# Kernel optimization log

Hardware: AMD Instinct MI355X
Metric: run time of the kernel (lower is better)

Reference implementation:

```python
import jax, jax.numpy as jnp
import numpy as np

B, L, H, A = 2, 1024, 768, 12          # batch, doc_len, hidden, attn heads
E, M, P = 24, 8, 552                   # entities/doc, mentions/entity, entity pairs/doc
EMB, BLK, NL = 768, 64, 97             # emb_size, block_size, num relation labels
OFFSET = 1                             # [CLS] offset


def setup_inputs() -> dict:
    key = jax.random.key(0)
    ks = jax.random.split(key, 16)
    w = lambda k, shape: (jax.random.normal(k, shape, jnp.float32) * 0.02)
    return {
        'sequence_output': jax.random.normal(ks[0], (B, L, H), jnp.float32),
        'attention': jax.random.uniform(ks[1], (B, A, L, L), jnp.float32),
        'mention_mask': jnp.ones((B, E, M), jnp.float32),
        'Wh': w(ks[2], (2 * H, EMB)),  'bh': jnp.zeros((EMB,), jnp.float32),
        'Wt': w(ks[3], (2 * H, EMB)),  'bt': jnp.zeros((EMB,), jnp.float32),
        'Wh2': w(ks[4], (3 * H, EMB)), 'bh2': jnp.zeros((EMB,), jnp.float32),
        'Wt2': w(ks[5], (3 * H, EMB)), 'bt2': jnp.zeros((EMB,), jnp.float32),
        'W2': w(ks[6], (EMB * BLK, H)), 'b2': jnp.zeros((H,), jnp.float32),
        'Wb': w(ks[7], (EMB * BLK, NL)), 'bb': jnp.zeros((NL,), jnp.float32),
        'mention_idx': jax.random.randint(ks[8], (B, E, M), 0, L - OFFSET),
        'hts': jax.random.randint(ks[9], (B, P, 2), 0, E),
    }


def _block_bilinear(a, b):
    # grouped (block) bilinear: [N, EMB] x [N, EMB] -> [N, EMB*BLK]
    b1 = a.reshape(-1, EMB // BLK, BLK)
    b2 = b.reshape(-1, EMB // BLK, BLK)
    return jnp.einsum('nkb,nkc->nkbc', b1, b2).reshape(-1, EMB * BLK)


def reference(sequence_output, attention, mention_mask,
              Wh, bh, Wt, bt, Wh2, bh2, Wt2, bt2, W2, b2, Wb, bb,
              mention_idx, hts):
    bidx = jnp.arange(B)[:, None, None]
    pos = mention_idx + OFFSET                              # [B,E,M]

    # --- get_hrt: ragged mention gather + logsumexp / mean pooling ---
    ment_emb = sequence_output[bidx, pos]                   # [B,E,M,H]
    mm = mention_mask[..., None]
    x = jnp.where(mm > 0, ment_emb, -1e30)
    mx = x.max(axis=2, keepdims=True)
    ent_emb = (mx + jnp.log(jnp.sum(jnp.exp(x - mx), axis=2, keepdims=True))).squeeze(2)  # [B,E,H]

    ment_att = attention[bidx, :, pos]                      # [B,E,M,A,L]
    cnt = jnp.clip(mention_mask.sum(-1), 1.0)[:, :, None, None]
    ent_att = (ment_att * mention_mask[..., None, None]).sum(2) / cnt  # [B,E,A,L]

    bidx2 = jnp.arange(B)[:, None]
    hs = ent_emb[bidx2, hts[..., 0]]                        # [B,P,H]
    ts = ent_emb[bidx2, hts[..., 1]]
    h_att = ent_att[bidx2, hts[..., 0]]                     # [B,P,A,L]
    t_att = ent_att[bidx2, hts[..., 1]]
    ht_att = (h_att * t_att).mean(2)                        # [B,P,L]
    ht_att = ht_att / (ht_att.sum(-1, keepdims=True) + 1e-30)
    rs = jnp.einsum('bpl,blh->bph', ht_att, sequence_output)  # localized context

    hs = hs.reshape(-1, H); ts = ts.reshape(-1, H); rs = rs.reshape(-1, H)

    # --- forward_rel: extractors + grouped block-bilinear scoring ---
    hs1 = jnp.tanh(jnp.concatenate([hs, rs], -1) @ Wh + bh)
    ts1 = jnp.tanh(jnp.concatenate([ts, rs], -1) @ Wt + bt)
    hts_feat = _block_bilinear(hs1, ts1) @ W2 + b2          # [N,H]
    hs2 = jnp.tanh(jnp.concatenate([hs1, rs, hts_feat], -1) @ Wh2 + bh2)
    ts2 = jnp.tanh(jnp.concatenate([ts1, rs, hts_feat], -1) @ Wt2 + bt2)
    logits = _block_bilinear(hs2, ts2) @ Wb + bb            # [N,NL]
    return logits
```

## Files before the change

### kernel.cpp

```cpp
#include <hip/hip_runtime.h>
#include <hip/hip_bf16.h>

#define B_ 2
#define L_ 1024
#define H_ 768
#define A_ 12
#define E_ 24
#define M_ 8
#define P_ 552
#define EMB_ 768
#define BLK_ 64
#define NBLK_ 12
#define NL_ 97
#define NP_ (B_*P_)
#define KTOT_ 49152
#define TP_ 8
#define NC_ 8

typedef float f32x4 __attribute__((ext_vector_type(4)));
typedef _Float16 f16x8 __attribute__((ext_vector_type(8)));

static __device__ __forceinline__ unsigned short f2h(float f){
    _Float16 h = (_Float16)f;
    unsigned short u; __builtin_memcpy(&u, &h, 2); return u;
}

static __device__ __forceinline__ void gload_lds16(const unsigned short* g, unsigned short* l){
    __builtin_amdgcn_global_load_lds(
        (const __attribute__((address_space(1))) unsigned int*)(const void*)g,
        (__attribute__((address_space(3))) unsigned int*)(void*)l, 16, 0, 0);
}

__global__ void k_ent_emb(const float* __restrict__ seq, const float* __restrict__ mask,
                          const int* __restrict__ midx, float* __restrict__ ent_emb)
{
    int be = blockIdx.x;
    int b = be / E_;
    int h = threadIdx.x;
    float v[M_];
    float mx = -1e30f;
    #pragma unroll
    for (int m = 0; m < M_; ++m) {
        float w = mask[be*M_ + m];
        int p = midx[be*M_ + m] + 1;
        float x = (w > 0.f) ? seq[(b*L_ + p)*H_ + h] : -1e30f;
        v[m] = x; mx = fmaxf(mx, x);
    }
    float s = 0.f;
    #pragma unroll
    for (int m = 0; m < M_; ++m) s += expf(v[m] - mx);
    ent_emb[be*H_ + h] = mx + logf(s);
}

__global__ void k_ent_att(const float* __restrict__ att, const float* __restrict__ mask,
                          const int* __restrict__ midx, float* __restrict__ ent_att)
{
    int bea = blockIdx.x;
    int a = bea % A_;
    int be = bea / A_;
    int b = be / E_;
    float cnt = 0.f;
    #pragma unroll
    for (int m = 0; m < M_; ++m) cnt += mask[be*M_ + m];
    cnt = fmaxf(cnt, 1.f);
    float inv = 1.f / cnt;
    for (int l = threadIdx.x; l < L_; l += blockDim.x) {
        float acc = 0.f;
        #pragma unroll
        for (int m = 0; m < M_; ++m) {
            float w = mask[be*M_ + m];
            if (w > 0.f) {
                int p = midx[be*M_ + m] + 1;
                acc += w * att[((size_t)(b*A_ + a)*L_ + p)*L_ + l];
            }
        }
        ent_att[(size_t)(be*A_ + a)*L_ + l] = acc * inv;
    }
}

__global__ void k_ht_att(const float* __restrict__ ent_att, const int* __restrict__ hts,
                         float* __restrict__ ht_att)
{
    int bp = blockIdx.x;
    int b = bp / P_;
    int he = hts[bp*2 + 0];
    int te = hts[bp*2 + 1];
    const float* ha = ent_att + (size_t)(b*E_ + he)*A_*L_;
    const float* ta = ent_att + (size_t)(b*E_ + te)*A_*L_;
    __shared__ float red[256];
    float lsum = 0.f;
    for (int l = threadIdx.x; l < L_; l += 256) {
        float q = 0.f;
        #pragma unroll
        for (int a = 0; a < A_; ++a) q += ha[a*L_ + l] * ta[a*L_ + l];
        q *= (1.f / A_);
        ht_att[(size_t)bp*L_ + l] = q;
        lsum += q;
    }
    red[threadIdx.x] = lsum;
    __syncthreads();
    for (int s = 128; s > 0; s >>= 1) {
        if (threadIdx.x < s) red[threadIdx.x] += red[threadIdx.x + s];
        __syncthreads();
    }
    float scale = 1.f / (red[0] + 1e-30f);
    for (int l = threadIdx.x; l < L_; l += 256)
        ht_att[(size_t)bp*L_ + l] *= scale;
}

__global__ void k_wt_multi(const float* __restrict__ W2, unsigned short* __restrict__ w2t,
                           const float* __restrict__ seq, unsigned short* __restrict__ seqT)
{
    int t = blockIdx.x;
    const float* in; unsigned short* out; int K, N, kt, ct;
    if (t < 9216)       { in = W2;              out = w2t;             K = KTOT_; N = 768; kt = t % 768; ct = t / 768; }
    else if (t < 9408)  { t -= 9216; in = seq;                 out = seqT;              K = L_; N = 768; kt = t % 16; ct = t / 16; }
    else                { t -= 9408; in = seq + (size_t)L_*H_; out = seqT + (size_t)768*L_; K = L_; N = 768; kt = t % 16; ct = t / 16; }
    __shared__ float tl[64][65];
    int k0 = kt*64, c0 = ct*64;
    int tx = threadIdx.x & 63, ty = threadIdx.x >> 6;
    #pragma unroll
    for (int q = 0; q < 16; ++q) {
        int r = ty*16 + q;
        tl[r][tx] = in[(size_t)(k0 + r)*N + c0 + tx];
    }
    __syncthreads();
    #pragma unroll
    for (int q = 0; q < 16; ++q) {
        int col = ty*16 + q;
        out[(size_t)(c0+col)*K + k0 + tx] = f2h(tl[tx][col]);
    }
}

__global__ void k_wt_f16(const float* __restrict__ in, unsigned short* __restrict__ out,
                         int K, int N, int Npad)
{
    __shared__ float t[64][65];
    int k0 = blockIdx.x*64, c0 = blockIdx.y*64;
    int tx = threadIdx.x & 63, ty = threadIdx.x >> 6;
    #pragma unroll
    for (int q = 0; q < 16; ++q) {
        int r = ty*16 + q;
        float v = 0.f;
        if (c0 + tx < N) v = in[(size_t)(k0 + r)*N + c0 + tx];
        t[r][tx] = v;
    }
    __syncthreads();
    #pragma unroll
    for (int q = 0; q < 16; ++q) {
        int col = ty*16 + q;
        if (c0 + col < Npad) out[(size_t)(c0+col)*K + k0 + tx] = f2h(t[tx][col]);
    }
}

__global__ void k_wt_f16x2(const float* __restrict__ in0, unsigned short* __restrict__ out0,
                           const float* __restrict__ in1, unsigned short* __restrict__ out1,
                           int K, int N, int Npad)
{
    const float* in = blockIdx.z ? in1 : in0;
    unsigned short* out = blockIdx.z ? out1 : out0;
    __shared__ float t[64][65];
    int k0 = blockIdx.x*64, c0 = blockIdx.y*64;
    int tx = threadIdx.x & 63, ty = threadIdx.x >> 6;
    #pragma unroll
    for (int q = 0; q < 16; ++q) {
        int r = ty*16 + q;
        float v = 0.f;
        if (c0 + tx < N) v = in[(size_t)(k0 + r)*N + c0 + tx];
        t[r][tx] = v;
    }
    __syncthreads();
    #pragma unroll
    for (int q = 0; q < 16; ++q) {
        int col = ty*16 + q;
        if (c0 + col < Npad) out[(size_t)(c0+col)*K + k0 + tx] = f2h(t[tx][col]);
    }
}

__launch_bounds__(256, 3)
__global__ void k_rs_mfma(const float* __restrict__ ht_att, const unsigned short* __restrict__ seqT,
                          float* __restrict__ Cpart)
{
    __shared__ _Float16 Ash[128][64];
    __shared__ _Float16 Bsh[128][64];
    int tid = threadIdx.x;
    int lane = tid & 63, wid = tid >> 6;
    int wr = (wid >> 1)*64, wc = (wid & 1)*64;
    int r16 = lane & 15, g = lane >> 4;
    int z = blockIdx.z;
    int b = z >> 3, kc = z & 7;
    int c0 = blockIdx.x*128;
    int row0 = blockIdx.y*128;
    const float* At = ht_att + (size_t)b*P_*L_;
    const unsigned short* Bt = seqT + (size_t)b*768*L_;
    int srccol = (lane >> 3);
    int srcch  = (lane & 7) ^ (srccol & 7);

    f32x4 acc[4][4];
    #pragma unroll
    for (int a = 0; a < 4; ++a)
        #pragma unroll
        for (int bq = 0; bq < 4; ++bq) acc[a][bq] = (f32x4){0.f,0.f,0.f,0.f};

    for (int s = 0; s < 2; ++s) {
        __syncthreads();
        #pragma unroll
        for (int q = 0; q < 4; ++q) {
            int idx = q*256 + tid;
            int row = idx >> 3, ch = idx & 7;
            int p = row0 + row; if (p >= P_) p = P_ - 1;
            const float* pp = &At[(size_t)p*L_ + kc*128 + s*64 + ch*8];
            f32x4 a0 = *(const f32x4*)pp;
            f32x4 a1 = *(const f32x4*)(pp + 4);
            f16x8 h;
            h[0]=(_Float16)a0[0]; h[1]=(_Float16)a0[1]; h[2]=(_Float16)a0[2]; h[3]=(_Float16)a0[3];
            h[4]=(_Float16)a1[0]; h[5]=(_Float16)a1[1]; h[6]=(_Float16)a1[2]; h[7]=(_Float16)a1[3];
            *(f16x8*)&Ash[row][(ch ^ (row & 7))*8] = h;
        }
        #pragma unroll
        for (int q = 0; q < 4; ++q) {
            int colb = (q*4 + wid)*8;
            int col = colb + srccol;
            gload_lds16(&Bt[(size_t)(c0+col)*L_ + kc*128 + s*64 + srcch*8],
                        (unsigned short*)&Bsh[colb][0]);
        }
        __syncthreads();
        #pragma unroll
        for (int kk = 0; kk < 2; ++kk) {
            f16x8 bfr[4];
            #pragma unroll
            for (int ni = 0; ni < 4; ++ni)
                bfr[ni] = *(f16x8*)&Bsh[wc + ni*16 + r16][((kk*4 + g) ^ (r16 & 7))*8];
            #pragma unroll
            for (int mi = 0; mi < 4; ++mi) {
                f16x8 afr = *(f16x8*)&Ash[wr + mi*16 + r16][((kk*4 + g) ^ (r16 & 7))*8];
                #pragma unroll
                for (int ni = 0; ni < 4; ++ni)
                    acc[mi][ni] = __builtin_amdgcn_mfma_f32_16x16x32_f16(afr, bfr[ni], acc[mi][ni], 0, 0, 0);
            }
        }
    }

    #pragma unroll
    for (int mi = 0; mi < 4; ++mi)
      #pragma unroll
      for (int ni = 0; ni < 4; ++ni)
        #pragma unroll
        for (int r = 0; r < 4; ++r) {
            int p = row0 + wr + mi*16 + g*4 + r;
            if (p < P_)
                Cpart[((size_t)kc*NP_ + b*P_ + p)*768 + c0 + wc + ni*16 + r16] = acc[mi][ni][r];
        }
}

__global__ void k_rs_reduce(const float* __restrict__ rspart, float* __restrict__ rs)
{
    int idx = blockIdx.x*256 + threadIdx.x;
    if (idx >= NP_*768/4) return;
    f32x4 s = {0.f,0.f,0.f,0.f};
    #pragma unroll
    for (int z = 0; z < NC_; ++z) s += *(const f32x4*)&rspart[(size_t)z*NP_*768 + (size_t)idx*4];
    *(f32x4*)&rs[(size_t)idx*4] = s;
}

__global__ void k_rs(const float* __restrict__ seq, const float* __restrict__ ht_att,
                     float* __restrict__ rs)
{
    int blk = blockIdx.x;
    int b = blk / (P_/TP_);
    int p0 = (blk % (P_/TP_)) * TP_;
    const float* sq = seq + (size_t)b*L_*H_;
    float acc[TP_][3];
    #pragma unroll
    for (int t = 0; t < TP_; ++t)
        #pragma unroll
        for (int c = 0; c < 3; ++c) acc[t][c] = 0.f;
    for (int l = 0; l < L_; ++l) {
        float w[TP_];
        #pragma unroll
        for (int t = 0; t < TP_; ++t) w[t] = ht_att[(size_t)(b*P_ + p0 + t)*L_ + l];
        #pragma unroll
        for (int c = 0; c < 3; ++c) {
            float v = sq[(size_t)l*H_ + threadIdx.x + 256*c];
            #pragma unroll
            for (int t = 0; t < TP_; ++t) acc[t][c] += w[t]*v;
        }
    }
    #pragma unroll
    for (int t = 0; t < TP_; ++t)
        #pragma unroll
        for (int c = 0; c < 3; ++c)
            rs[(size_t)(b*P_ + p0 + t)*H_ + threadIdx.x + 256*c] = acc[t][c];
}

__global__ void k_gather(const float* __restrict__ ent_emb, const int* __restrict__ hts,
                         float* __restrict__ hs, float* __restrict__ ts)
{
    int bp = blockIdx.x;
    int b = bp / P_;
    int he = hts[bp*2 + 0];
    int te = hts[bp*2 + 1];
    int h = threadIdx.x;
    hs[(size_t)bp*H_ + h] = ent_emb[(b*E_ + he)*H_ + h];
    ts[(size_t)bp*H_ + h] = ent_emb[(b*E_ + te)*H_ + h];
}

__global__ void k_gemm_reduce_tanh2(const float* __restrict__ gpA, const float* __restrict__ gpB,
                                    const float* __restrict__ biasA, const float* __restrict__ biasB,
                                    float* __restrict__ CA, float* __restrict__ CB, int nz)
{
    const float* Cpart = blockIdx.y ? gpB : gpA;
    const float* bias  = blockIdx.y ? biasB : biasA;
    float* C           = blockIdx.y ? CB : CA;
    int idx = blockIdx.x*256 + threadIdx.x;
    if (idx >= NP_*768/4) return;
    int c4 = (idx*4) % 768;
    f32x4 s = *(const f32x4*)&bias[c4];
    for (int z = 0; z < nz; ++z) s += *(const f32x4*)&Cpart[(size_t)z*NP_*768 + (size_t)idx*4];
    f32x4 r;
    #pragma unroll
    for (int j = 0; j < 4; ++j) r[j] = tanhf(s[j]);
    *(f32x4*)&C[(size_t)idx*4] = r;
}

template<int NPARTS, bool DOTANH>
__global__ void k_gemm_concat(const float* __restrict__ A0, const float* __restrict__ A1,
                              const float* __restrict__ A2, const float* __restrict__ W,
                              const float* __restrict__ bias, float* __restrict__ C,
                              int Mrows)
{
    const int BK = 16;
    __shared__ float As[BK][64];
    __shared__ float Bs[BK][64];
    int tid = threadIdx.x;
    int ty = tid >> 4, tx = tid & 15;
    int by = blockIdx.y, bx = blockIdx.x;
    float acc[4][4] = {};
    const int K = NPARTS * 768;
    for (int kk0 = 0; kk0 < K; kk0 += BK) {
        const float* Ap = (kk0 < 768) ? A0 : ((NPARTS >= 3 && kk0 >= 1536) ? A2 : A1);
        int klocal = kk0 % 768;
        {
            int idx = tid * 4;
            int r = idx >> 4;
            int k = idx & 15;
            int row = by*64 + r;
            float4 v = make_float4(0.f,0.f,0.f,0.f);
            if (row < Mrows) v = *(const float4*)(Ap + (size_t)row*768 + klocal + k);
            As[k+0][r] = v.x; As[k+1][r] = v.y; As[k+2][r] = v.z; As[k+3][r] = v.w;
        }
        {
            int idx = tid * 4;
            int k = idx >> 6;
            int c = idx & 63;
            *(float4*)&Bs[k][c] = *(const float4*)(W + (size_t)(kk0 + k)*768 + bx*64 + c);
        }
        __syncthreads();
        #pragma unroll
        for (int k = 0; k < BK; ++k) {
            float a4[4], b4[4];
            *(float4*)a4 = *(float4*)&As[k][ty*4];
            *(float4*)b4 = *(float4*)&Bs[k][tx*4];
            #pragma unroll
            for (int i = 0; i < 4; ++i)
                #pragma unroll
                for (int j = 0; j < 4; ++j) acc[i][j] += a4[i]*b4[j];
        }
        __syncthreads();
    }
    #pragma unroll
    for (int i = 0; i < 4; ++i) {
        int row = by*64 + ty*4 + i;
        if (row >= Mrows) continue;
        #pragma unroll
        for (int j = 0; j < 4; ++j) {
            int col = bx*64 + tx*4 + j;
            float v = acc[i][j] + bias[col];
            if (DOTANH) v = tanhf(v);
            C[(size_t)row*768 + col] = v;
        }
    }
}

template<int NSTEP, bool GATHER0>
__launch_bounds__(256, 3)
__global__ void k_gemm_mfma2(const float* __restrict__ A0a, const float* __restrict__ A0b,
                             const float* __restrict__ A1, const float* __restrict__ A2,
                             const int* __restrict__ hts,
                             const unsigned short* __restrict__ WTa, const unsigned short* __restrict__ WTb,
                             float* __restrict__ Cpa, float* __restrict__ Cpb,
                             int Mrows, int Ktot, int partdiv, int nzhalf)
{
    __shared__ _Float16 Ash[128][64];
    __shared__ _Float16 Bsh[128][64];
    int tid = threadIdx.x;
    int lane = tid & 63, wid = tid >> 6;
    int wr = (wid >> 1)*64, wc = (wid & 1)*64;
    int r16 = lane & 15, g = lane >> 4;
    int zz = blockIdx.z;
    int half = zz / nzhalf;
    int z = zz % nzhalf;
    const unsigned short* WT = half ? WTb : WTa;
    float* Cpart = half ? Cpb : Cpa;
    int part = z / partdiv, chunk = z % partdiv;
    int ka = chunk * (NSTEP*64);
    int kb = part*768 + ka;
    const float* A = (part == 0) ? (half ? A0b : A0a) : ((part == 1) ? A1 : A2);
    int c0 = blockIdx.x*128;
    int row0 = blockIdx.y*128;
    int srccol = (lane >> 3);
    int srcch  = (lane & 7) ^ (srccol & 7);

    f32x4 acc[4][4];
    #pragma unroll
    for (int a = 0; a < 4; ++a)
        #pragma unroll
        for (int b = 0; b < 4; ++b) acc[a][b] = (f32x4){0.f,0.f,0.f,0.f};

    for (int s = 0; s < NSTEP; ++s) {
        __syncthreads();
        #pragma unroll
        for (int q = 0; q < 4; ++q) {
            int idx = q*256 + tid;
            int row = idx >> 3, ch = idx & 7;
            int grow = row0 + row; if (grow >= Mrows) grow = Mrows - 1;
            const float* p;
            if (GATHER0 && part == 0) {
                int bb_ = grow / P_;
                int e = hts[grow*2 + half];
                p = &A0a[((size_t)(bb_*E_ + e))*768 + ka + s*64 + ch*8];
            } else {
                p = &A[(size_t)grow*768 + ka + s*64 + ch*8];
            }
            f32x4 a0 = *(const f32x4*)p;
            f32x4 a1 = *(const f32x4*)(p + 4);
            f16x8 h;
            h[0]=(_Float16)a0[0]; h[1]=(_Float16)a0[1]; h[2]=(_Float16)a0[2]; h[3]=(_Float16)a0[3];
            h[4]=(_Float16)a1[0]; h[5]=(_Float16)a1[1]; h[6]=(_Float16)a1[2]; h[7]=(_Float16)a1[3];
            *(f16x8*)&Ash[row][(ch ^ (row & 7))*8] = h;
        }
        #pragma unroll
        for (int q = 0; q < 4; ++q) {
            int colb = (q*4 + wid)*8;
            int col = colb + srccol;
            gload_lds16(&WT[(size_t)(c0+col)*Ktot + kb + s*64 + srcch*8],
                        (unsigned short*)&Bsh[colb][0]);
        }
        __syncthreads();
        #pragma unroll
        for (int kk = 0; kk < 2; ++kk) {
            f16x8 bfr[4];
            #pragma unroll
            for (int ni = 0; ni < 4; ++ni)
                bfr[ni] = *(f16x8*)&Bsh[wc + ni*16 + r16][((kk*4 + g) ^ (r16 & 7))*8];
            #pragma unroll
            for (int mi = 0; mi < 4; ++mi) {
                f16x8 afr = *(f16x8*)&Ash[wr + mi*16 + r16][((kk*4 + g) ^ (r16 & 7))*8];
                #pragma unroll
                for (int ni = 0; ni < 4; ++ni)
                    acc[mi][ni] = __builtin_amdgcn_mfma_f32_16x16x32_f16(afr, bfr[ni], acc[mi][ni], 0, 0, 0);
            }
        }
    }

    #pragma unroll
    for (int mi = 0; mi < 4; ++mi)
      #pragma unroll
      for (int ni = 0; ni < 4; ++ni)
        #pragma unroll
        for (int r = 0; r < 4; ++r) {
            int row = row0 + wr + mi*16 + g*4 + r;
            if (row < Mrows)
                Cpart[((size_t)z*Mrows + row)*768 + c0 + wc + ni*16 + r16] = acc[mi][ni][r];
        }
}

template<int ILEN, bool SWZ>
__launch_bounds__(256, 3)
__global__ void k_bb_mfma(const float* __restrict__ U, const float* __restrict__ V,
                          const unsigned short* __restrict__ BT, float* __restrict__ Cpart,
                          int Mrows, int ldc)
{
    const int ISPLIT = 64 / ILEN;
    __shared__ unsigned short Ush[128][ILEN + 2];
    __shared__ _Float16 Bs[2][128][64];
    int tid = threadIdx.x;
    int lane = tid & 63, wid = tid >> 6;
    int wr = (wid >> 1)*64, wc = (wid & 1)*64;
    int r16 = lane & 15, g = lane >> 4;
    int bx = blockIdx.x, by = blockIdx.y, z = blockIdx.z;
    if (SWZ) {
        int h = bx + 6*by + 54*z;
        int x = h & 7, j = h >> 3;
        int p = x*9 + j/9;
        by = j % 9;
        bx = p % 6;
        z  = p / 6;
    }
    int kz = z / ISPLIT, si = z % ISPLIT;
    int ibeg = si * ILEN;
    int c0 = bx*128;
    int row0 = by*128;
    int srccol = (lane >> 3);
    int srcch  = (lane & 7) ^ (srccol & 7);
    const unsigned short* BTkz = BT + (size_t)kz*4096;

    #pragma unroll
    for (int q = 0; q < (128*ILEN)/1024; ++q) {
        int idx = (q*256 + tid)*4;
        int r = idx / ILEN, c = idx % ILEN;
        int row = row0 + r; if (row >= Mrows) row = Mrows - 1;
        f32x4 v = *(const f32x4*)&U[(size_t)row*EMB_ + kz*64 + ibeg + c];
        Ush[r][c+0] = f2h(v[0]); Ush[r][c+1] = f2h(v[1]);
        Ush[r][c+2] = f2h(v[2]); Ush[r][c+3] = f2h(v[3]);
    }
    f16x8 vfh[2][4];
    #pragma unroll
    for (int kk = 0; kk < 2; ++kk)
      #pragma unroll
      for (int mi = 0; mi < 4; ++mi) {
        int row = row0 + wr + mi*16 + r16; if (row >= Mrows) row = Mrows - 1;
        const float* p = &V[(size_t)row*EMB_ + kz*64 + kk*32 + g*8];
        f16x8 t;
        #pragma unroll
        for (int e = 0; e < 8; ++e) t[e] = (_Float16)p[e];
        vfh[kk][mi] = t;
      }
    #pragma unroll
    for (int q = 0; q < 4; ++q) {
        int colb = (q*4 + wid)*8;
        int col = colb + srccol;
        gload_lds16(&BTkz[(size_t)(c0+col)*KTOT_ + (size_t)ibeg*64 + srcch*8],
                    (unsigned short*)&Bs[0][colb][0]);
    }
    __syncthreads();

    f32x4 acc[4][4];
    #pragma unroll
    for (int a = 0; a < 4; ++a)
        #pragma unroll
        for (int b = 0; b < 4; ++b) acc[a][b] = (f32x4){0.f,0.f,0.f,0.f};

    for (int ii = 0; ii < ILEN; ++ii) {
        int cur = ii & 1, nxt = cur ^ 1;
        if (ii < ILEN-1) {
            #pragma unroll
            for (int q = 0; q < 4; ++q) {
                int colb = (q*4 + wid)*8;
                int col = colb + srccol;
                gload_lds16(&BTkz[(size_t)(c0+col)*KTOT_ + (size_t)(ibeg+ii+1)*64 + srcch*8],
                            (unsigned short*)&Bs[nxt][colb][0]);
            }
        }
        f16x8 u8[4];
        #pragma unroll
        for (int mi = 0; mi < 4; ++mi) {
            unsigned short ub = Ush[wr + mi*16 + r16][ii];
            _Float16 uh; __builtin_memcpy(&uh, &ub, 2);
            #pragma unroll
            for (int e = 0; e < 8; ++e) u8[mi][e] = uh;
        }
        #pragma unroll
        for (int kk = 0; kk < 2; ++kk) {
            f16x8 bfr[4];
            #pragma unroll
            for (int ni = 0; ni < 4; ++ni) {
                int row = wc + ni*16 + r16;
                bfr[ni] = *(f16x8*)&Bs[cur][row][((kk*4 + g) ^ (r16 & 7))*8];
            }
            #pragma unroll
            for (int mi = 0; mi < 4; ++mi) {
                f16x8 afr = u8[mi] * vfh[kk][mi];
                #pragma unroll
                for (int ni = 0; ni < 4; ++ni)
                    acc[mi][ni] = __builtin_amdgcn_mfma_f32_16x16x32_f16(afr, bfr[ni], acc[mi][ni], 0, 0, 0);
            }
        }
        __syncthreads();
    }

    #pragma unroll
    for (int mi = 0; mi < 4; ++mi)
      #pragma unroll
      for (int ni = 0; ni < 4; ++ni)
        #pragma unroll
        for (int r = 0; r < 4; ++r) {
            int row = row0 + wr + mi*16 + g*4 + r;
            if (row < Mrows)
                Cpart[((size_t)z*Mrows + row)*ldc + c0 + wc + ni*16 + r16] = acc[mi][ni][r];
        }
}

__global__ void k_reduce_feat(const float* __restrict__ part, const float* __restrict__ bias,
                              float* __restrict__ out)
{
    int idx = blockIdx.x*256 + threadIdx.x;
    if (idx >= (NP_*768)/4) return;
    int c4 = (idx*4) % 768;
    f32x4 s = *(const f32x4*)&bias[c4];
    #pragma unroll
    for (int z = 0; z < NBLK_; ++z) s += *(const f32x4*)&part[(size_t)z*NP_*768 + (size_t)idx*4];
    *(f32x4*)&out[(size_t)idx*4] = s;
}

__global__ void k_reduce_logits(const float* __restrict__ part, const float* __restrict__ bb,
                                float* __restrict__ out, int nz)
{
    int idx = blockIdx.x*256 + threadIdx.x;
    if (idx >= NP_*NL_) return;
    int n = idx / NL_, c = idx % NL_;
    float s = bb[c];
    for (int z = 0; z < nz; ++z) s += part[(size_t)z*NP_*128 + (size_t)n*128 + c];
    out[idx] = s;
}

template<bool GUARD, bool SPLITK>
__global__ void k_bbgemm(const float* __restrict__ U, const float* __restrict__ V,
                         const float* __restrict__ W, const float* __restrict__ bias,
                         float* __restrict__ C, int Mrows, int Ncols, int ldw, int ldc)
{
    __shared__ float Us[64][68];
    __shared__ float Vs[64][68];
    __shared__ float Bsh[16][64];
    int tid = threadIdx.x;
    int ty = tid >> 4, tx = tid & 15;
    int by = blockIdx.y, bx = blockIdx.x;
    int c0 = bx*64;
    float acc[4][4] = {};
    int kbeg = SPLITK ? blockIdx.z : 0;
    int kend = SPLITK ? blockIdx.z + 1 : NBLK_;
    for (int k = kbeg; k < kend; ++k) {
        #pragma unroll
        for (int e = 0; e < 4; ++e) {
            int idx = (e*256 + tid)*4;
            int r = idx >> 6, c = idx & 63;
            int row = by*64 + r;
            float4 u = make_float4(0.f,0.f,0.f,0.f), vv = make_float4(0.f,0.f,0.f,0.f);
            if (row < Mrows) {
                u  = *(const float4*)(U + (size_t)row*EMB_ + k*BLK_ + c);
                vv = *(const float4*)(V + (size_t)row*EMB_ + k*BLK_ + c);
            }
            *(float4*)&Us[r][c] = u;
            *(float4*)&Vs[r][c] = vv;
        }
        __syncthreads();
        for (int t = 0; t < 256; ++t) {
            int i = t >> 2;
            int jb = (t & 3) * 16;
            {
                int idx = tid * 4;
                int kk = idx >> 6, c = idx & 63;
                size_t wrow = (size_t)(k*256 + t)*16 + kk;
                if (GUARD) {
                    #pragma unroll
                    for (int q = 0; q < 4; ++q) {
                        int col = c0 + c + q;
                        Bsh[kk][c+q] = (col < Ncols) ? W[wrow*ldw + col] : 0.f;
                    }
                } else {
                    *(float4*)&Bsh[kk][c] = *(const float4*)(W + wrow*ldw + c0 + c);
                }
            }
            __syncthreads();
            float u[4];
            #pragma unroll
            for (int r = 0; r < 4; ++r) u[r] = Us[ty*4+r][i];
            #pragma unroll
            for (int kk = 0; kk < 16; ++kk) {
                float b4[4];
                *(float4*)b4 = *(float4*)&Bsh[kk][tx*4];
                #pragma unroll
                for (int r = 0; r < 4; ++r) {
                    float a = u[r] * Vs[ty*4+r][jb+kk];
                    #pragma unroll
                    for (int j = 0; j < 4; ++j) acc[r][j] += a*b4[j];
                }
            }
            __syncthreads();
        }
    }
    #pragma unroll
    for (int r = 0; r < 4; ++r) {
        int row = by*64 + ty*4 + r;
        if (row >= Mrows) continue;
        #pragma unroll
        for (int j = 0; j < 4; ++j) {
            int col = c0 + tx*4 + j;
            if (GUARD && col >= Ncols) continue;
            float v = acc[r][j];
            if (!SPLITK) v += bias[col];
            size_t out_idx = SPLITK ? ((size_t)(blockIdx.z*Mrows + row)*ldc + col)
                                    : ((size_t)row*ldc + col);
            C[out_idx] = v;
        }
    }
}

__global__ void k_logits_reduce_old(const float* __restrict__ part, const float* __restrict__ bb,
                                    float* __restrict__ out)
{
    int idx = blockIdx.x*256 + threadIdx.x;
    if (idx >= NP_*NL_) return;
    int col = idx % NL_;
    float s = bb[col];
    #pragma unroll
    for (int z = 0; z < NBLK_; ++z) s += part[(size_t)z*NP_*NL_ + idx];
    out[idx] = s;
}

extern "C" void kernel_launch(void* const* d_in, const int* in_sizes, int n_in,
                              void* d_out, int out_size, void* d_ws, size_t ws_size,
                              hipStream_t stream)
{
    (void)in_sizes; (void)n_in; (void)out_size;
    const float* seq  = (const float*)d_in[0];
    const float* att  = (const float*)d_in[1];
    const float* mask = (const float*)d_in[2];
    const float* Wh   = (const float*)d_in[3];
    const float* bh   = (const float*)d_in[4];
    const float* Wt   = (const float*)d_in[5];
    const float* bt   = (const float*)d_in[6];
    const float* Wh2  = (const float*)d_in[7];
    const float* bh2  = (const float*)d_in[8];
    const float* Wt2  = (const float*)d_in[9];
    const float* bt2  = (const float*)d_in[10];
    const float* W2   = (const float*)d_in[11];
    const float* b2   = (const float*)d_in[12];
    const float* Wb   = (const float*)d_in[13];
    const float* bb   = (const float*)d_in[14];
    const int* midx   = (const int*)d_in[15];
    const int* hts    = (const int*)d_in[16];
    float* out = (float*)d_out;
    float* ws  = (float*)d_ws;

    float* ent_emb = ws;
    float* ent_att = ent_emb + 36864;
    float* ht_att  = ent_att + 589824;
    float* rs      = ht_att + 1130496;
    float* hs      = rs   + 847872;
    float* ts      = hs   + 847872;
    float* hs1     = ts   + 847872;
    float* ts1     = hs1  + 847872;
    float* feat    = ts1  + 847872;
    float* hs2     = feat + 847872;
    float* ts2     = hs2  + 847872;
    float* featpart = ts2 + 847872;
    float* spare    = featpart + 10174464;
    unsigned short* w2t = (unsigned short*)(spare + 1695744);
    unsigned short* Rrgn = (unsigned short*)(spare + 1695744 + 18874368);
    const size_t need_bytes = (size_t)42430464 * 4;
    const bool use_mfma = (ws_size >= need_bytes);

    unsigned short* whT  = Rrgn;
    unsigned short* wtT  = Rrgn + 1179648;
    unsigned short* wh2T = Rrgn;
    unsigned short* wt2T = Rrgn + 1769472;
    unsigned short* wbt  = Rrgn;

    unsigned short* seqT = (unsigned short*)hs;

    float* rspart  = featpart;
    float* gpA     = featpart;
    float* gpB     = featpart + 5087232;
    float* logpart = featpart;

    k_ent_emb<<<dim3(B_*E_), dim3(H_), 0, stream>>>(seq, mask, midx, ent_emb);
    k_ent_att<<<dim3(B_*E_*A_), dim3(256), 0, stream>>>(att, mask, midx, ent_att);
    k_ht_att<<<dim3(NP_), dim3(256), 0, stream>>>(ent_att, hts, ht_att);

    if (use_mfma) {
        k_wt_multi<<<dim3(9600), dim3(256), 0, stream>>>(W2, w2t, seq, seqT);

        k_rs_mfma<<<dim3(6, 5, 16), dim3(256), 0, stream>>>(ht_att, seqT, rspart);
        k_rs_reduce<<<dim3(828), dim3(256), 0, stream>>>(rspart, rs);

        k_wt_f16x2<<<dim3(1536/64, 768/64, 2), dim3(256), 0, stream>>>(Wh, whT, Wt, wtT, 1536, 768, 768);

        k_gemm_mfma2<4, true><<<dim3(6, 9, 12), dim3(256), 0, stream>>>(
            ent_emb, ent_emb, rs, rs, hts, whT, wtT, gpA, gpB, NP_, 1536, 3, 6);
        k_gemm_reduce_tanh2<<<dim3(828, 2), dim3(256), 0, stream>>>(gpA, gpB, bh, bt, hs1, ts1, 6);

        k_bb_mfma<64, true><<<dim3(6, 9, NBLK_), dim3(256), 0, stream>>>(hs1, ts1, w2t, featpart, NP_, 768);
        k_reduce_feat<<<dim3((NP_*768/4 + 255)/256), dim3(256), 0, stream>>>(featpart, b2, feat);

        k_wt_f16x2<<<dim3(2304/64, 768/64, 2), dim3(256), 0, stream>>>(Wh2, wh2T, Wt2, wt2T, 2304, 768, 768);

        k_gemm_mfma2<6, false><<<dim3(6, 9, 12), dim3(256), 0, stream>>>(
            hs1, ts1, rs, feat, hts, wh2T, wt2T, gpA, gpB, NP_, 2304, 2, 6);
        k_gemm_reduce_tanh2<<<dim3(828, 2), dim3(256), 0, stream>>>(gpA, gpB, bh2, bt2, hs2, ts2, 6);

        k_wt_f16<<<dim3(KTOT_/64, 128/64), dim3(256), 0, stream>>>(Wb, wbt, KTOT_, NL_, 128);
        k_bb_mfma<16, false><<<dim3(1, 9, NBLK_*4), dim3(256), 0, stream>>>(hs2, ts2, wbt, logpart, NP_, 128);
        k_reduce_logits<<<dim3((NP_*NL_ + 255)/256), dim3(256), 0, stream>>>(logpart, bb, out, NBLK_*4);
    } else {
        k_rs<<<dim3(B_*(P_/TP_)), dim3(256), 0, stream>>>(seq, ht_att, rs);
        k_gather<<<dim3(NP_), dim3(H_), 0, stream>>>(ent_emb, hts, hs, ts);
        dim3 gg(12, (NP_+63)/64);
        k_gemm_concat<2, true><<<gg, dim3(256), 0, stream>>>(hs, rs, nullptr, Wh, bh, hs1, NP_);
        k_gemm_concat<2, true><<<gg, dim3(256), 0, stream>>>(ts, rs, nullptr, Wt, bt, ts1, NP_);
        float* lpart = featpart;
        k_bbgemm<false, false><<<gg, dim3(256), 0, stream>>>(hs1, ts1, W2, b2, feat, NP_, 768, 768, 768);
        k_gemm_concat<3, true><<<gg, dim3(256), 0, stream>>>(hs1, rs, feat, Wh2, bh2, hs2, NP_);
        k_gemm_concat<3, true><<<gg, dim3(256), 0, stream>>>(ts1, rs, feat, Wt2, bt2, ts2, NP_);
        k_bbgemm<true, true><<<dim3(2, (NP_+63)/64, NBLK_), dim3(256), 0, stream>>>(
            hs2, ts2, Wb, nullptr, lpart, NP_, NL_, NL_, NL_);
        k_logits_reduce_old<<<dim3((NP_*NL_ + 255)/256), dim3(256), 0, stream>>>(lpart, bb, out);
    }
}
```

Baseline: 323.3 us.

## Fold weight transposes into one launch and deepen bilinear MFMA prefetch pipeline

Merges the Wh, Wt and Wb fp16 transposes into the existing multi-transpose kernel, removing two separate launches. To keep those buffers alive, the transposed weights are moved into otherwise dead workspace regions. The block-bilinear MFMA kernel now prefetches two stages ahead with explicit vmcnt waits and raw barriers instead of a full __syncthreads per iteration. It also loads U values eight at a time as a vector from padded LDS. This adds aliasing risk if any reused region is still live, and the hand-written waitcnt logic is fragile.

```diff
diff --git a/kernel.cpp b/kernel.cpp
--- a/kernel.cpp
+++ b/kernel.cpp
@@ -109,47 +109,35 @@
 }
 
 __global__ void k_wt_multi(const float* __restrict__ W2, unsigned short* __restrict__ w2t,
-                           const float* __restrict__ seq, unsigned short* __restrict__ seqT)
+                           const float* __restrict__ seq, unsigned short* __restrict__ seqT,
+                           const float* __restrict__ Wh, unsigned short* __restrict__ whT,
+                           const float* __restrict__ Wt, unsigned short* __restrict__ wtT,
+                           const float* __restrict__ Wb, unsigned short* __restrict__ wbt)
 {
     int t = blockIdx.x;
-    const float* in; unsigned short* out; int K, N, kt, ct;
-    if (t < 9216)       { in = W2;              out = w2t;             K = KTOT_; N = 768; kt = t % 768; ct = t / 768; }
-    else if (t < 9408)  { t -= 9216; in = seq;                 out = seqT;              K = L_; N = 768; kt = t % 16; ct = t / 16; }
-    else                { t -= 9408; in = seq + (size_t)L_*H_; out = seqT + (size_t)768*L_; K = L_; N = 768; kt = t % 16; ct = t / 16; }
+    const float* in; unsigned short* out; int K, N, kt, ct; bool guard = false;
+    if (t < 9216)       { in = W2; out = w2t; K = KTOT_; N = 768; kt = t % 768; ct = t / 768; }
+    else if (t < 9600)  { t -= 9216; int b = t / 192; t %= 192;
+                          in = seq + (size_t)b*L_*H_; out = seqT + (size_t)b*768*L_;
+                          K = L_; N = 768; kt = t % 16; ct = t / 16; }
+    else if (t < 9888)  { t -= 9600;  in = Wh; out = whT; K = 1536; N = 768; kt = t % 24; ct = t / 24; }
+    else if (t < 10176) { t -= 9888;  in = Wt; out = wtT; K = 1536; N = 768; kt = t % 24; ct = t / 24; }
+    else                { t -= 10176; in = Wb; out = wbt; K = KTOT_; N = NL_; kt = t % 768; ct = t / 768; guard = true; }
     __shared__ float tl[64][65];
     int k0 = kt*64, c0 = ct*64;
     int tx = threadIdx.x & 63, ty = threadIdx.x >> 6;
     #pragma unroll
     for (int q = 0; q < 16; ++q) {
         int r = ty*16 + q;
-        tl[r][tx] = in[(size_t)(k0 + r)*N + c0 + tx];
+        float v = 0.f;
+        if (!guard || (c0 + tx < N)) v = in[(size_t)(k0 + r)*N + c0 + tx];
+        tl[r][tx] = v;
     }
     __syncthreads();
     #pragma unroll
     for (int q = 0; q < 16; ++q) {
         int col = ty*16 + q;
         out[(size_t)(c0+col)*K + k0 + tx] = f2h(tl[tx][col]);
-    }
-}
-
-__global__ void k_wt_f16(const float* __restrict__ in, unsigned short* __restrict__ out,
-                         int K, int N, int Npad)
-{
-    __shared__ float t[64][65];
-    int k0 = blockIdx.x*64, c0 = blockIdx.y*64;
-    int tx = threadIdx.x & 63, ty = threadIdx.x >> 6;
-    #pragma unroll
-    for (int q = 0; q < 16; ++q) {
-        int r = ty*16 + q;
-        float v = 0.f;
-        if (c0 + tx < N) v = in[(size_t)(k0 + r)*N + c0 + tx];
-        t[r][tx] = v;
-    }
-    __syncthreads();
-    #pragma unroll
-    for (int q = 0; q < 16; ++q) {
-        int col = ty*16 + q;
-        if (c0 + col < Npad) out[(size_t)(c0+col)*K + k0 + tx] = f2h(t[tx][col]);
     }
 }
 
@@ -482,7 +470,7 @@
                           int Mrows, int ldc)
 {
     const int ISPLIT = 64 / ILEN;
-    __shared__ unsigned short Ush[128][ILEN + 2];
+    __shared__ unsigned short Ush[128][ILEN + 8];
     __shared__ _Float16 Bs[2][128][64];
     int tid = threadIdx.x;
     int lane = tid & 63, wid = tid >> 6;
@@ -533,7 +521,15 @@
         gload_lds16(&BTkz[(size_t)(c0+col)*KTOT_ + (size_t)ibeg*64 + srcch*8],
                     (unsigned short*)&Bs[0][colb][0]);
     }
-    __syncthreads();
+    #pragma unroll
+    for (int q = 0; q < 4; ++q) {
+        int colb = (q*4 + wid)*8;
+        int col = colb + srccol;
+        gload_lds16(&BTkz[(size_t)(c0+col)*KTOT_ + (size_t)(ibeg+1)*64 + srcch*8],
+                    (unsigned short*)&Bs[1][colb][0]);
+    }
+    asm volatile("s_waitcnt vmcnt(4) lgkmcnt(0)" ::: "memory");
+    __builtin_amdgcn_s_barrier();
 
     f32x4 acc[4][4];
     #pragma unroll
@@ -541,42 +537,54 @@
         #pragma unroll
         for (int b = 0; b < 4; ++b) acc[a][b] = (f32x4){0.f,0.f,0.f,0.f};
 
-    for (int ii = 0; ii < ILEN; ++ii) {
-        int cur = ii & 1, nxt = cur ^ 1;
-        if (ii < ILEN-1) {
-            #pragma unroll
-            for (int q = 0; q < 4; ++q) {
-                int colb = (q*4 + wid)*8;
-                int col = colb + srccol;
-                gload_lds16(&BTkz[(size_t)(c0+col)*KTOT_ + (size_t)(ibeg+ii+1)*64 + srcch*8],
-                            (unsigned short*)&Bs[nxt][colb][0]);
-            }
-        }
-        f16x8 u8[4];
-        #pragma unroll
-        for (int mi = 0; mi < 4; ++mi) {
-            unsigned short ub = Ush[wr + mi*16 + r16][ii];
-            _Float16 uh; __builtin_memcpy(&uh, &ub, 2);
-            #pragma unroll
-            for (int e = 0; e < 8; ++e) u8[mi][e] = uh;
-        }
-        #pragma unroll
-        for (int kk = 0; kk < 2; ++kk) {
-            f16x8 bfr[4];
-            #pragma unroll
-            for (int ni = 0; ni < 4; ++ni) {
-                int row = wc + ni*16 + r16;
-                bfr[ni] = *(f16x8*)&Bs[cur][row][((kk*4 + g) ^ (r16 & 7))*8];
-            }
+    for (int i8 = 0; i8 < ILEN/8; ++i8) {
+        f16x8 ureg[4];
+        #pragma unroll
+        for (int mi = 0; mi < 4; ++mi)
+            ureg[mi] = *(const f16x8*)&Ush[wr + mi*16 + r16][i8*8];
+        #pragma unroll
+        for (int e = 0; e < 8; ++e) {
+            int ii = i8*8 + e;
+            int cur = ii & 1;
+            f16x8 u8[4];
             #pragma unroll
             for (int mi = 0; mi < 4; ++mi) {
-                f16x8 afr = u8[mi] * vfh[kk][mi];
+                _Float16 uh = ureg[mi][e];
                 #pragma unroll
-                for (int ni = 0; ni < 4; ++ni)
-                    acc[mi][ni] = __builtin_amdgcn_mfma_f32_16x16x32_f16(afr, bfr[ni], acc[mi][ni], 0, 0, 0);
-            }
-        }
-        __syncthreads();
+                for (int q2 = 0; q2 < 8; ++q2) u8[mi][q2] = uh;
+            }
+            #pragma unroll
+            for (int kk = 0; kk < 2; ++kk) {
+                f16x8 bfr[4];
+                #pragma unroll
+                for (int ni = 0; ni < 4; ++ni) {
+                    int row = wc + ni*16 + r16;
+                    bfr[ni] = *(f16x8*)&Bs[cur][row][((kk*4 + g) ^ (r16 & 7))*8];
+                }
+                #pragma unroll
+                for (int mi = 0; mi < 4; ++mi) {
+                    f16x8 afr = u8[mi] * vfh[kk][mi];
+                    #pragma unroll
+                    for (int ni = 0; ni < 4; ++ni)
+                        acc[mi][ni] = __builtin_amdgcn_mfma_f32_16x16x32_f16(afr, bfr[ni], acc[mi][ni], 0, 0, 0);
+                }
+            }
+            __builtin_amdgcn_s_barrier();
+            if (ii + 2 < ILEN) {
+                #pragma unroll
+                for (int q = 0; q < 4; ++q) {
+                    int colb = (q*4 + wid)*8;
+                    int col = colb + srccol;
+                    gload_lds16(&BTkz[(size_t)(c0+col)*KTOT_ + (size_t)(ibeg+ii+2)*64 + srcch*8],
+                                (unsigned short*)&Bs[cur][colb][0]);
+                }
+            }
+            if (ii + 1 < ILEN) {
+                if (ii + 2 < ILEN) { asm volatile("s_waitcnt vmcnt(4)" ::: "memory"); }
+                else               { asm volatile("s_waitcnt vmcnt(0)" ::: "memory"); }
+                __builtin_amdgcn_s_barrier();
+            }
+        }
     }
 
     #pragma unroll
@@ -751,12 +759,11 @@
     const size_t need_bytes = (size_t)42430464 * 4;
     const bool use_mfma = (ws_size >= need_bytes);
 
-    unsigned short* whT  = Rrgn;
-    unsigned short* wtT  = Rrgn + 1179648;
-    unsigned short* wh2T = Rrgn;
-    unsigned short* wt2T = Rrgn + 1769472;
+    unsigned short* whT  = (unsigned short*)ent_att;
+    unsigned short* wtT  = (unsigned short*)ts;
+    unsigned short* wh2T = (unsigned short*)ht_att;
+    unsigned short* wt2T = (unsigned short*)spare;
     unsigned short* wbt  = Rrgn;
-
     unsigned short* seqT = (unsigned short*)hs;
 
     float* rspart  = featpart;
@@ -769,12 +776,11 @@
     k_ht_att<<<dim3(NP_), dim3(256), 0, stream>>>(ent_att, hts, ht_att);
 
     if (use_mfma) {
-        k_wt_multi<<<dim3(9600), dim3(256), 0, stream>>>(W2, w2t, seq, seqT);
+        k_wt_multi<<<dim3(11712), dim3(256), 0, stream>>>(W2, w2t, seq, seqT,
+                                                          Wh, whT, Wt, wtT, Wb, wbt);
 
         k_rs_mfma<<<dim3(6, 5, 16), dim3(256), 0, stream>>>(ht_att, seqT, rspart);
         k_rs_reduce<<<dim3(828), dim3(256), 0, stream>>>(rspart, rs);
-
-        k_wt_f16x2<<<dim3(1536/64, 768/64, 2), dim3(256), 0, stream>>>(Wh, whT, Wt, wtT, 1536, 768, 768);
 
         k_gemm_mfma2<4, true><<<dim3(6, 9, 12), dim3(256), 0, stream>>>(
             ent_emb, ent_emb, rs, rs, hts, whT, wtT, gpA, gpB, NP_, 1536, 3, 6);
@@ -789,7 +795,6 @@
             hs1, ts1, rs, feat, hts, wh2T, wt2T, gpA, gpB, NP_, 2304, 2, 6);
         k_gemm_reduce_tanh2<<<dim3(828, 2), dim3(256), 0, stream>>>(gpA, gpB, bh2, bt2, hs2, ts2, 6);
 
-        k_wt_f16<<<dim3(KTOT_/64, 128/64), dim3(256), 0, stream>>>(Wb, wbt, KTOT_, NL_, 128);
         k_bb_mfma<16, false><<<dim3(1, 9, NBLK_*4), dim3(256), 0, stream>>>(hs2, ts2, wbt, logpart, NP_, 128);
         k_reduce_logits<<<dim3((NP_*NL_ + 255)/256), dim3(256), 0, stream>>>(logpart, bb, out, NBLK_*4);
     } else {
```

After: 337.9 us. 1.05x slower.
